# Kernel tuning notes

Hardware: AMD Instinct MI355X
Metric: run time of the kernel (lower is better)

The kernel has to match this reference:

```python
import jax, jax.numpy as jnp
import numpy as np

S, B, D, H = 2048, 2, 1024, 16
DK = D // H


def rotate_half(x):
    # interleaved variant: pairs (x0,x1)->(-x1,x0)
    x1 = x[..., ::2]
    x2 = x[..., 1::2]
    return jnp.stack((-x2, x1), axis=-1).reshape(x.shape)


def apply_rope(x):
    # x: [B, H, S, dk]
    b, h, s, dk = x.shape
    pos = jnp.arange(s, dtype=jnp.float32)
    inv_freq = 1.0 / (10000.0 ** (jnp.arange(0, dk, 2, dtype=jnp.float32) / dk))
    freqs = jnp.einsum('i,j->ij', pos, inv_freq)          # [S, dk/2]
    emb = jnp.concatenate((freqs, freqs), axis=-1)        # [S, dk]  (non-interleaved cos/sin, as in source)
    cos = jnp.cos(emb)[None, None, :, :]
    sin = jnp.sin(emb)[None, None, :, :]
    return x * cos + rotate_half(x) * sin


def setup_inputs() -> dict:
    key = jax.random.key(0)
    ks = jax.random.split(key, 11)
    sc = 0.02
    return {
        'query': jax.random.normal(ks[0], (S, B, D), jnp.float32),
        'key':   jax.random.normal(ks[1], (S, B, D), jnp.float32),
        'value': jax.random.normal(ks[2], (S, B, D), jnp.float32),
        'wq': jax.random.normal(ks[3], (D, D), jnp.float32) * sc,
        'bq': jax.random.normal(ks[4], (D,), jnp.float32) * sc,
        'wk': jax.random.normal(ks[5], (D, D), jnp.float32) * sc,
        'bk': jax.random.normal(ks[6], (D,), jnp.float32) * sc,
        'wv': jax.random.normal(ks[7], (D, D), jnp.float32) * sc,
        'bv': jax.random.normal(ks[8], (D,), jnp.float32) * sc,
        'wo': jax.random.normal(ks[9], (D, D), jnp.float32) * sc,
        'bo': jax.random.normal(ks[10], (D,), jnp.float32) * sc,
    }


def reference(query, key, value, wq, bq, wk, bk, wv, bv, wo, bo):
    s_q, b, _ = query.shape
    s_k = key.shape[0]

    def split_heads(x, s):
        # [S,B,D] -> [B,H,S,dk]
        return x.transpose(1, 0, 2).reshape(b, s, H, DK).transpose(0, 2, 1, 3)

    Q = split_heads(query @ wq.T + bq, s_q)
    K = split_heads(key @ wk.T + bk, s_k)
    V = split_heads(value @ wv.T + bv, s_k)

    Q = apply_rope(Q)
    K = apply_rope(K)

    scores = jnp.einsum('bhqd,bhkd->bhqk', Q, K) / jnp.sqrt(jnp.float32(DK))
    attn = jax.nn.softmax(scores, axis=-1)
    out = jnp.einsum('bhqk,bhkd->bhqd', attn, V)          # [B,H,Sq,dk]
    out = out.transpose(0, 2, 1, 3).reshape(b, s_q, D)    # [B,Sq,D]
    out = out.transpose(1, 0, 2)                          # [Sq,B,D]
    return out @ wo.T + bo
```

## Files before the change

### kernel.cpp

```cpp
#include <hip/hip_runtime.h>
#include <cstdint>
#include <cstddef>

typedef __attribute__((ext_vector_type(4))) float f32x4;
typedef __attribute__((ext_vector_type(8))) float f32x8;
typedef __attribute__((ext_vector_type(16))) float f32x16;
typedef __attribute__((ext_vector_type(8))) __bf16 bf16x8;
typedef __attribute__((ext_vector_type(4))) __bf16 bf16x4;
typedef __attribute__((ext_vector_type(2))) __bf16 bf16x2;
typedef __attribute__((ext_vector_type(4))) unsigned int u32x4;
typedef unsigned short u16;

#define S_LEN 2048
#define BATCH 2
#define DMODEL 1024
#define NHEAD 16
#define HDK 64

__device__ __forceinline__ u16 f2bf(float f) {
    uint32_t u = __float_as_uint(f);
    u += 0x7FFFu + ((u >> 16) & 1u);
    return (u16)(u >> 16);
}

__device__ __forceinline__ void gload_lds16(const void* g, void* l) {
    __builtin_amdgcn_global_load_lds(
        (const __attribute__((address_space(1))) uint32_t*)g,
        (__attribute__((address_space(3))) uint32_t*)l, 16, 0, 0);
}

__device__ __forceinline__ unsigned pk2(float a, float b) {
    bf16x2 t;
    t[0] = (__bf16)a; t[1] = (__bf16)b;
    return __builtin_bit_cast(unsigned, t);
}

__device__ __forceinline__ float fmax3(float a, float b, float c) {
    return fmaxf(fmaxf(a, b), c);
}

__device__ __forceinline__ f32x16 z16() {
    f32x16 v = {0.f,0.f,0.f,0.f,0.f,0.f,0.f,0.f,0.f,0.f,0.f,0.f,0.f,0.f,0.f,0.f};
    return v;
}

__global__ __launch_bounds__(256) void cvt_kernel(
    const float* __restrict__ a0, const float* __restrict__ a1, const float* __restrict__ a2,
    const float* __restrict__ a3, const float* __restrict__ a4, const float* __restrict__ a5,
    const float* __restrict__ a6,
    u16* __restrict__ o0, u16* __restrict__ o1, u16* __restrict__ o2,
    u16* __restrict__ o3, u16* __restrict__ o4, u16* __restrict__ o5,
    u16* __restrict__ o6)
{
    const int by = blockIdx.y;
    const float* s;
    u16* d;
    int n;
    switch (by) {
        case 0: s = a0; d = o0; n = 4194304; break;
        case 1: s = a1; d = o1; n = 4194304; break;
        case 2: s = a2; d = o2; n = 4194304; break;
        case 3: s = a3; d = o3; n = 1048576; break;
        case 4: s = a4; d = o4; n = 1048576; break;
        case 5: s = a5; d = o5; n = 1048576; break;
        default: s = a6; d = o6; n = 1048576; break;
    }
    int idx = (blockIdx.x * 256 + threadIdx.x) * 8;
    if (idx >= n) return;
    float4 f0 = *(const float4*)(s + idx);
    float4 f1 = *(const float4*)(s + idx + 4);
    alignas(16) u16 o[8] = {f2bf(f0.x), f2bf(f0.y), f2bf(f0.z), f2bf(f0.w),
                            f2bf(f1.x), f2bf(f1.y), f2bf(f1.z), f2bf(f1.w)};
    *(u32x4*)(d + idx) = *(const u32x4*)o;
}

__global__ __launch_bounds__(512, 6) void qkv_kernel(
    const u16* __restrict__ X0, const u16* __restrict__ X1, const u16* __restrict__ X2,
    const u16* __restrict__ W0, const u16* __restrict__ W1, const u16* __restrict__ W2,
    const float* __restrict__ B0, const float* __restrict__ B1, const float* __restrict__ B2,
    u16* __restrict__ O0, u16* __restrict__ O1, u16* __restrict__ O2)
{
    __shared__ __align__(16) u16 lA[2][128 * 32];
    __shared__ __align__(16) u16 lB[2][128 * 32];
    const int tid = threadIdx.x, wid = tid >> 6, lane = tid & 63;
    const int l15 = lane & 15, l4 = lane >> 4;
    const int p = blockIdx.y * 32 + blockIdx.x;
    const int vid = (p & 7) * 96 + (p >> 3);
    const int bx = vid & 31, byv = vid >> 5;
    const int mat = byv >> 3;
    const u16* X = mat == 0 ? X0 : (mat == 1 ? X1 : X2);
    const u16* W = mat == 0 ? W0 : (mat == 1 ? W1 : W2);
    const float* bias = mat == 0 ? B0 : (mat == 1 ? B1 : B2);
    u16* O = mat == 0 ? O0 : (mat == 1 ? O1 : O2);
    const int m0 = bx * 128, n0 = (byv & 7) * 128;
    const int mw = (wid >> 1) * 32, nw = (wid & 1) * 64;

    f32x4 acc[2][4];
#pragma unroll
    for (int i = 0; i < 2; ++i)
#pragma unroll
        for (int j = 0; j < 4; ++j) acc[i][j] = (f32x4){0.f, 0.f, 0.f, 0.f};

    const int srow = tid >> 2, sg = (tid & 3) ^ (srow & 3);

#define QSTAGE(bufi, k0_) do {                                                \
        gload_lds16(X + (size_t)(m0 + srow) * 1024 + (k0_) + sg * 8,          \
                    (char*)lA + (bufi) * 8192 + (tid & ~63) * 16);            \
        gload_lds16(W + (size_t)(n0 + srow) * 1024 + (k0_) + sg * 8,          \
                    (char*)lB + (bufi) * 8192 + (tid & ~63) * 16);            \
    } while (0)

    QSTAGE(0, 0);
    for (int ks = 0; ks < 32; ++ks) {
        const int cur = ks & 1;
        if (ks < 31) {
            QSTAGE(cur ^ 1, (ks + 1) * 32);
            asm volatile("s_waitcnt vmcnt(2)" ::: "memory");
        } else {
            asm volatile("s_waitcnt vmcnt(0)" ::: "memory");
        }
        __builtin_amdgcn_s_barrier();
        const char* la = (const char*)lA + cur * 8192;
        const char* lb = (const char*)lB + cur * 8192;
        __builtin_amdgcn_s_setprio(1);
        bf16x8 af[2], bfr[4];
#pragma unroll
        for (int f = 0; f < 2; ++f) {
            int ra = mw + f * 16 + l15;
            af[f] = *(const bf16x8*)(la + ra * 64 +
                    ((l4 * 16) ^ ((ra & 3) << 4)));
        }
#pragma unroll
        for (int f = 0; f < 4; ++f) {
            int rb = nw + f * 16 + l15;
            bfr[f] = *(const bf16x8*)(lb + rb * 64 +
                    ((l4 * 16) ^ ((rb & 3) << 4)));
        }
#pragma unroll
        for (int mf = 0; mf < 2; ++mf)
#pragma unroll
            for (int nf = 0; nf < 4; ++nf)
                acc[mf][nf] = __builtin_amdgcn_mfma_f32_16x16x32_bf16(
                    af[mf], bfr[nf], acc[mf][nf], 0, 0, 0);
        __builtin_amdgcn_s_setprio(0);
        __builtin_amdgcn_s_barrier();
    }
#undef QSTAGE

#pragma unroll
    for (int mf = 0; mf < 2; ++mf) {
#pragma unroll
        for (int nf = 0; nf < 4; ++nf) {
            int gcol = n0 + nw + nf * 16 + l15;
            float bval = bias[gcol];
            int h = gcol >> 6, d = gcol & 63;
            float invf = __expf(-(float)(d & 31) * 0.2878231366f);
#pragma unroll
            for (int i = 0; i < 4; ++i) {
                int grow = m0 + mw + mf * 16 + l4 * 4 + i;
                int s = grow >> 1, b = grow & 1;
                float v = acc[mf][nf][i] + bval;
                if (mat < 2) {
                    float p2 = __shfl_xor(v, 1);
                    float th = (float)s * invf;
                    float sn, cs;
                    __sincosf(th, &sn, &cs);
                    v = (d & 1) ? fmaf(p2, sn, v * cs) : fmaf(-p2, sn, v * cs);
                    if (mat == 0) v *= 0.18033688f;
                }
                O[((size_t)(b * NHEAD + h) * S_LEN + s) * HDK + d] = f2bf(v);
            }
        }
    }
}

__global__ __launch_bounds__(256) void vtrans_kernel(const u16* __restrict__ Vr, u16* __restrict__ Vt)
{
    __shared__ __align__(16) u16 t[64][72];
    const int tid = threadIdx.x, bh = blockIdx.y, s0 = blockIdx.x * 64;
    const u16* src = Vr + (size_t)bh * S_LEN * HDK;
    u16* dst = Vt + (size_t)bh * HDK * S_LEN;
    int r = tid >> 2, cbase = (tid & 3) * 16;
#pragma unroll
    for (int j = 0; j < 2; ++j)
        *(bf16x8*)&t[r][cbase + j * 8] =
            *(const bf16x8*)(const void*)(src + (size_t)(s0 + r) * HDK + cbase + j * 8);
    __syncthreads();
    int d = tid >> 2;
#pragma unroll
    for (int j = 0; j < 2; ++j) {
        alignas(16) u16 tmp[8];
#pragma unroll
        for (int x = 0; x < 8; ++x) {
            int lp = j * 8 + x;
            int sl = (lp & 3) | ((lp & 4) << 1) | ((lp & 8) >> 1);
            tmp[x] = t[cbase + sl][d];
        }
        *(bf16x8*)(void*)(dst + (size_t)d * S_LEN + s0 + cbase + j * 8) = *(const bf16x8*)tmp;
    }
}

__global__ __launch_bounds__(512, 4) void attn_kernel(
    const u16* __restrict__ Q, const u16* __restrict__ K,
    const u16* __restrict__ V, u16* __restrict__ O)
{
    __shared__ __align__(16) char smem[65536];
    const int tid = threadIdx.x, wid = tid >> 6, lane = tid & 63;
    const int g = wid >> 2, wv = wid & 3;
    const int l31 = lane & 31, hi = lane >> 5;
    const int p = blockIdx.y * 16 + blockIdx.x;
    const int vid = (p & 7) * 64 + (p >> 3);
    const int bh = vid >> 4, b = bh >> 4, h = bh & 15;
    const int q0 = (vid & 15) * 128;
    const u16* Qb = Q + (size_t)bh * S_LEN * HDK;
    const u16* Kb = K + (size_t)bh * S_LEN * HDK;
    const u16* Vb = V + (size_t)bh * HDK * S_LEN;

    const int qrow = q0 + wv * 32 + l31;
    bf16x8 aq[4];
#pragma unroll
    for (int ks = 0; ks < 4; ++ks)
        aq[ks] = *(const bf16x8*)(const void*)(Qb + (size_t)qrow * HDK + ks * 16 + hi * 8);

    f32x16 acc0 = z16(), acc1 = z16();
    float mrow = -1e30f, lpart = 0.f;

    char* gbase = smem + g * 32768;
    const int gt = tid & 255;
    const int srow = gt >> 3, lg = (gt & 7) ^ (srow & 7);
    char* sK = gbase + wv * 1024;
    char* sV = gbase + 8192 + wv * 1024;
    const u16* pk0 = Kb + (size_t)(g * 1024 + srow) * HDK + lg * 8;
    const u16* pk1 = pk0 + 32 * HDK;
    const u16* pv0 = Vb + (size_t)srow * S_LEN + g * 1024 + lg * 8;
    const u16* pv1 = pv0 + (size_t)32 * S_LEN;

    const int swl = (l31 & 7) << 4;
    const char* akr[4];
    const char* avr[4];
#pragma unroll
    for (int i = 0; i < 4; ++i) {
        akr[i] = gbase + l31 * 128 + ((i * 32 + hi * 16) ^ swl);
        avr[i] = gbase + 8192 + l31 * 128 + ((i * 32 + hi * 16) ^ swl);
    }

    gload_lds16(pk0, sK);
    gload_lds16(pk1, sK + 4096);
    gload_lds16(pv0, sV);
    gload_lds16(pv1, sV + 4096);
    pk0 += 4096; pk1 += 4096; pv0 += 64; pv1 += 64;

#define TILE(CUR_, STG_) do {                                                 \
    if (STG_) {                                                               \
        gload_lds16(pk0, sK + ((CUR_) ^ 1) * 16384);                          \
        gload_lds16(pk1, sK + ((CUR_) ^ 1) * 16384 + 4096);                   \
        gload_lds16(pv0, sV + ((CUR_) ^ 1) * 16384);                          \
        gload_lds16(pv1, sV + ((CUR_) ^ 1) * 16384 + 4096);                   \
        pk0 += 4096; pk1 += 4096; pv0 += 64; pv1 += 64;                       \
        asm volatile("s_waitcnt vmcnt(4)" ::: "memory");                      \
    } else {                                                                  \
        asm volatile("s_waitcnt vmcnt(0)" ::: "memory");                      \
    }                                                                         \
    __builtin_amdgcn_s_barrier();                                             \
    f32x16 s0 = z16(), s1 = z16();                                            \
    __builtin_amdgcn_s_setprio(1);                                            \
    _Pragma("unroll")                                                         \
    for (int ks = 0; ks < 4; ++ks) {                                          \
        bf16x8 a0 = *(const bf16x8*)(akr[ks] + (CUR_) * 16384);               \
        bf16x8 a1 = *(const bf16x8*)(akr[ks] + (CUR_) * 16384 + 4096);        \
        s0 = __builtin_amdgcn_mfma_f32_32x32x16_bf16(a0, aq[ks], s0, 0, 0, 0);\
        s1 = __builtin_amdgcn_mfma_f32_32x32x16_bf16(a1, aq[ks], s1, 0, 0, 0);\
    }                                                                         \
    __builtin_amdgcn_s_setprio(0);                                            \
    float a0_ = fmax3(s0[0], s0[1], s0[2]);                                   \
    float a1_ = fmax3(s0[3], s0[4], s0[5]);                                   \
    float a2_ = fmax3(s0[6], s0[7], s0[8]);                                   \
    float a3_ = fmax3(s0[9], s0[10], s0[11]);                                 \
    float a4_ = fmax3(s0[12], s0[13], s0[14]);                                \
    float b0_ = fmax3(s1[0], s1[1], s1[2]);                                   \
    float b1_ = fmax3(s1[3], s1[4], s1[5]);                                   \
    float b2_ = fmax3(s1[6], s1[7], s1[8]);                                   \
    float b3_ = fmax3(s1[9], s1[10], s1[11]);                                 \
    float b4_ = fmax3(s1[12], s1[13], s1[14]);                                \
    float t0_ = fmax3(a0_, a1_, a2_);                                         \
    float t1_ = fmax3(a3_, a4_, s0[15]);                                      \
    float t2_ = fmax3(b0_, b1_, b2_);                                         \
    float t3_ = fmax3(b3_, b4_, s1[15]);                                      \
    float pmax = fmaxf(fmax3(t0_, t1_, t2_), t3_);                            \
    pmax = fmaxf(pmax, __shfl_xor(pmax, 32));                                 \
    if (!__all(pmax - mrow <= 11.5f)) {                                       \
        float mn = fmaxf(mrow, pmax);                                         \
        float sc = __builtin_amdgcn_exp2f(mrow - mn);                         \
        lpart *= sc;                                                          \
        acc0 *= sc; acc1 *= sc;                                               \
        mrow = mn;                                                            \
    }                                                                         \
    _Pragma("unroll")                                                         \
    for (int i = 0; i < 16; ++i) {                                            \
        s0[i] = __builtin_amdgcn_exp2f(s0[i] - mrow);                         \
        s1[i] = __builtin_amdgcn_exp2f(s1[i] - mrow);                         \
    }                                                                         \
    {                                                                         \
        f32x16 sm_ = s0 + s1;                                                 \
        f32x8 q8_ = __builtin_shufflevector(sm_, sm_, 0,1,2,3,4,5,6,7)        \
                  + __builtin_shufflevector(sm_, sm_, 8,9,10,11,12,13,14,15); \
        f32x4 q4_ = __builtin_shufflevector(q8_, q8_, 0,1,2,3)                \
                  + __builtin_shufflevector(q8_, q8_, 4,5,6,7);               \
        lpart += (q4_[0] + q4_[1]) + (q4_[2] + q4_[3]);                       \
    }                                                                         \
    __builtin_amdgcn_s_setprio(1);                                            \
    _Pragma("unroll")                                                         \
    for (int i = 0; i < 4; ++i) {                                             \
        const f32x16* cp = (i >> 1) ? &s1 : &s0;                              \
        const int e0 = (i & 1) * 8;                                           \
        u32x4 bw;                                                             \
        bw[0] = pk2((*cp)[e0 + 0], (*cp)[e0 + 1]);                            \
        bw[1] = pk2((*cp)[e0 + 2], (*cp)[e0 + 3]);                            \
        bw[2] = pk2((*cp)[e0 + 4], (*cp)[e0 + 5]);                            \
        bw[3] = pk2((*cp)[e0 + 6], (*cp)[e0 + 7]);                            \
        bf16x8 Bf = __builtin_bit_cast(bf16x8, bw);                           \
        bf16x8 av0 = *(const bf16x8*)(avr[i] + (CUR_) * 16384);               \
        bf16x8 av1 = *(const bf16x8*)(avr[i] + (CUR_) * 16384 + 4096);        \
        acc0 = __builtin_amdgcn_mfma_f32_32x32x16_bf16(av0, Bf, acc0, 0, 0, 0);\
        acc1 = __builtin_amdgcn_mfma_f32_32x32x16_bf16(av1, Bf, acc1, 0, 0, 0);\
    }                                                                         \
    __builtin_amdgcn_s_setprio(0);                                            \
    __builtin_amdgcn_s_barrier();                                             \
} while (0)

    for (int th = 0; th < 8; ++th) {
        TILE(0, 1);
        TILE(1, (th < 7));
    }
#undef TILE

    lpart += __shfl_xor(lpart, 32);
    float* exO = (float*)smem;
    float* exML = (float*)(smem + 36864);
    const int sl = wv * 64 + lane;
    if (g == 1) {
#pragma unroll
        for (int r4 = 0; r4 < 4; ++r4) {
            f32x4 w0 = {acc0[r4 * 4 + 0], acc0[r4 * 4 + 1], acc0[r4 * 4 + 2], acc0[r4 * 4 + 3]};
            f32x4 w1 = {acc1[r4 * 4 + 0], acc1[r4 * 4 + 1], acc1[r4 * 4 + 2], acc1[r4 * 4 + 3]};
            *(f32x4*)(exO + sl * 36 + r4 * 4) = w0;
            *(f32x4*)(exO + sl * 36 + 16 + r4 * 4) = w1;
        }
        exML[sl * 2] = mrow;
        exML[sl * 2 + 1] = lpart;
    }
    __syncthreads();
    if (g == 0) {
        float m1 = exML[sl * 2], l1 = exML[sl * 2 + 1];
        float mm = fmaxf(mrow, m1);
        float f0 = __builtin_amdgcn_exp2f(mrow - mm);
        float f1 = __builtin_amdgcn_exp2f(m1 - mm);
        float rl = 1.0f / (lpart * f0 + l1 * f1);
        f0 *= rl; f1 *= rl;
        u16* obase = O + ((size_t)qrow * BATCH + b) * DMODEL + h * HDK;
#pragma unroll
        for (int db = 0; db < 2; ++db) {
#pragma unroll
            for (int r4 = 0; r4 < 4; ++r4) {
                f32x4 part = *(const f32x4*)(exO + sl * 36 + db * 16 + r4 * 4);
                bf16x4 outv;
#pragma unroll
                for (int e = 0; e < 4; ++e) {
                    float own = db ? acc1[r4 * 4 + e] : acc0[r4 * 4 + e];
                    outv[e] = (__bf16)(own * f0 + part[e] * f1);
                }
                *(bf16x4*)(void*)(obase + db * 32 + 8 * r4 + 4 * hi) = outv;
            }
        }
    }
}

__global__ __launch_bounds__(256) void proj_kernel(
    const u16* __restrict__ A, const u16* __restrict__ W,
    const float* __restrict__ bias, float* __restrict__ out)
{
    __shared__ __align__(16) u16 lA[2][64 * 64];
    __shared__ __align__(16) u16 lB[2][128 * 64];
    const int tid = threadIdx.x, wid = tid >> 6, lane = tid & 63;
    const int l15 = lane & 15, l4 = lane >> 4;
    const int p = blockIdx.y * 8 + blockIdx.x;
    const int vid = (p & 7) * 64 + (p >> 3);
    const int m0 = (vid & 63) * 64, n0 = (vid >> 6) * 128;
    const int nw = wid * 32;

    f32x4 acc[4][2];
#pragma unroll
    for (int i = 0; i < 4; ++i)
#pragma unroll
        for (int j = 0; j < 2; ++j) acc[i][j] = (f32x4){0.f, 0.f, 0.f, 0.f};

#define PSTAGE(bufi, k0_) do {                                                \
        _Pragma("unroll")                                                     \
        for (int it = 0; it < 2; ++it) {                                      \
            int cc = it * 256 + tid;                                          \
            int row = cc >> 3, gg = (cc & 7) ^ (row & 7);                     \
            gload_lds16(A + (size_t)(m0 + row) * 1024 + (k0_) + gg * 8,       \
                        (char*)lA + (bufi) * 8192 + (cc & ~63) * 16);         \
        }                                                                     \
        _Pragma("unroll")                                                     \
        for (int it = 0; it < 4; ++it) {                                      \
            int cc = it * 256 + tid;                                          \
            int row = cc >> 3, gg = (cc & 7) ^ (row & 7);                     \
            gload_lds16(W + (size_t)(n0 + row) * 1024 + (k0_) + gg * 8,       \
                        (char*)lB + (bufi) * 16384 + (cc & ~63) * 16);        \
        }                                                                     \
    } while (0)

    PSTAGE(0, 0);
    for (int ks = 0; ks < 16; ++ks) {
        const int cur = ks & 1;
        if (ks < 15) {
            PSTAGE(cur ^ 1, (ks + 1) * 64);
            asm volatile("s_waitcnt vmcnt(6)" ::: "memory");
        } else {
            asm volatile("s_waitcnt vmcnt(0)" ::: "memory");
        }
        __builtin_amdgcn_s_barrier();
        const char* la = (const char*)lA + cur * 8192;
        const char* lb = (const char*)lB + cur * 16384;
        __builtin_amdgcn_s_setprio(1);
#pragma unroll
        for (int kk = 0; kk < 2; ++kk) {
            bf16x8 af[4], bfr[2];
#pragma unroll
            for (int f = 0; f < 4; ++f) {
                int ra = f * 16 + l15;
                af[f] = *(const bf16x8*)(la + ra * 128 +
                        ((kk * 64 + l4 * 16) ^ ((ra & 7) << 4)));
            }
#pragma unroll
            for (int f = 0; f < 2; ++f) {
                int rb = nw + f * 16 + l15;
                bfr[f] = *(const bf16x8*)(lb + rb * 128 +
                        ((kk * 64 + l4 * 16) ^ ((rb & 7) << 4)));
            }
#pragma unroll
            for (int mf = 0; mf < 4; ++mf)
#pragma unroll
                for (int nf = 0; nf < 2; ++nf)
                    acc[mf][nf] = __builtin_amdgcn_mfma_f32_16x16x32_bf16(
                        af[mf], bfr[nf], acc[mf][nf], 0, 0, 0);
        }
        __builtin_amdgcn_s_setprio(0);
        __builtin_amdgcn_s_barrier();
    }
#undef PSTAGE

#pragma unroll
    for (int mf = 0; mf < 4; ++mf) {
#pragma unroll
        for (int nf = 0; nf < 2; ++nf) {
            int gcol = n0 + nw + nf * 16 + l15;
            float bval = bias[gcol];
#pragma unroll
            for (int i = 0; i < 4; ++i) {
                int grow = m0 + mf * 16 + l4 * 4 + i;
                out[(size_t)grow * DMODEL + gcol] = acc[mf][nf][i] + bval;
            }
        }
    }
}

extern "C" void kernel_launch(void* const* d_in, const int* in_sizes, int n_in,
                              void* d_out, int out_size, void* d_ws, size_t ws_size,
                              hipStream_t stream)
{
    (void)in_sizes; (void)n_in; (void)out_size; (void)ws_size;
    const float* q  = (const float*)d_in[0];
    const float* k  = (const float*)d_in[1];
    const float* v  = (const float*)d_in[2];
    const float* wq = (const float*)d_in[3];
    const float* bq = (const float*)d_in[4];
    const float* wk = (const float*)d_in[5];
    const float* bk = (const float*)d_in[6];
    const float* wv = (const float*)d_in[7];
    const float* bv = (const float*)d_in[8];
    const float* wo = (const float*)d_in[9];
    const float* bo = (const float*)d_in[10];

    char* ws = (char*)d_ws;
    const size_t MB = 1024 * 1024;
    u16* XQ  = (u16*)(ws + 0 * MB);
    u16* XK  = (u16*)(ws + 8 * MB);
    u16* XV  = (u16*)(ws + 16 * MB);
    u16* WQb = (u16*)(ws + 24 * MB);
    u16* WKb = (u16*)(ws + 26 * MB);
    u16* WVb = (u16*)(ws + 28 * MB);
    u16* WOb = (u16*)(ws + 30 * MB);
    u16* QR  = (u16*)(ws + 32 * MB);
    u16* KR  = (u16*)(ws + 40 * MB);
    u16* VR  = (u16*)(ws + 48 * MB);
    u16* VT  = XK;
    u16* OA  = XQ;

    cvt_kernel<<<dim3(2048, 7), 256, 0, stream>>>(q, k, v, wq, wk, wv, wo,
                                                  XQ, XK, XV, WQb, WKb, WVb, WOb);
    qkv_kernel<<<dim3(32, 24), 512, 0, stream>>>(XQ, XK, XV, WQb, WKb, WVb,
                                                 bq, bk, bv, QR, KR, VR);
    vtrans_kernel<<<dim3(32, 32), 256, 0, stream>>>(VR, VT);
    attn_kernel<<<dim3(16, 32), 512, 0, stream>>>(QR, KR, VT, OA);
    proj_kernel<<<dim3(8, 64), 256, 0, stream>>>(OA, WOb, bo, (float*)d_out);
}
```

Before: 125.1 us.

## Drop intra-block KV split in attention and use post-exp lazy rescaling

The attention kernel no longer splits the KV sequence between two 4-wave groups in a 512-thread block. Each 256-thread block now walks the whole KV length, which removes the cross-group LDS merge and its block-wide sync and halves shared memory per block. The online softmax now exponentiates scores against a fixed running offset first, and rescales only when a tile's exponentiated max exceeds a threshold, using a reciprocal and log2. In exchange, each block runs twice as many serial KV tiles with half the waves, so per-block latency rises. The new rescaling scheme also carries overflow and precision risk if scores jump by a large amount within a single tile.

After: 129.0 us. +3.0%, slower.

```diff
diff --git a/kernel.cpp b/kernel.cpp
--- a/kernel.cpp
+++ b/kernel.cpp
@@ -200,13 +200,12 @@
     }
 }
 
-__global__ __launch_bounds__(512, 4) void attn_kernel(
+__global__ __launch_bounds__(256) void attn_kernel(
     const u16* __restrict__ Q, const u16* __restrict__ K,
     const u16* __restrict__ V, u16* __restrict__ O)
 {
-    __shared__ __align__(16) char smem[65536];
+    __shared__ __align__(16) char smem[32768];
     const int tid = threadIdx.x, wid = tid >> 6, lane = tid & 63;
-    const int g = wid >> 2, wv = wid & 3;
     const int l31 = lane & 31, hi = lane >> 5;
     const int p = blockIdx.y * 16 + blockIdx.x;
     const int vid = (p & 7) * 64 + (p >> 3);
@@ -216,23 +215,21 @@
     const u16* Kb = K + (size_t)bh * S_LEN * HDK;
     const u16* Vb = V + (size_t)bh * HDK * S_LEN;
 
-    const int qrow = q0 + wv * 32 + l31;
+    const int qrow = q0 + wid * 32 + l31;
     bf16x8 aq[4];
 #pragma unroll
     for (int ks = 0; ks < 4; ++ks)
         aq[ks] = *(const bf16x8*)(const void*)(Qb + (size_t)qrow * HDK + ks * 16 + hi * 8);
 
     f32x16 acc0 = z16(), acc1 = z16();
-    float mrow = -1e30f, lpart = 0.f;
-
-    char* gbase = smem + g * 32768;
-    const int gt = tid & 255;
-    const int srow = gt >> 3, lg = (gt & 7) ^ (srow & 7);
-    char* sK = gbase + wv * 1024;
-    char* sV = gbase + 8192 + wv * 1024;
-    const u16* pk0 = Kb + (size_t)(g * 1024 + srow) * HDK + lg * 8;
+    float mrow = 0.0f, lpart = 0.f;
+
+    const int srow = tid >> 3, lg = (tid & 7) ^ (srow & 7);
+    char* sK = smem + wid * 1024;
+    char* sV = smem + 8192 + wid * 1024;
+    const u16* pk0 = Kb + (size_t)srow * HDK + lg * 8;
     const u16* pk1 = pk0 + 32 * HDK;
-    const u16* pv0 = Vb + (size_t)srow * S_LEN + g * 1024 + lg * 8;
+    const u16* pv0 = Vb + (size_t)srow * S_LEN + lg * 8;
     const u16* pv1 = pv0 + (size_t)32 * S_LEN;
 
     const int swl = (l31 & 7) << 4;
@@ -240,8 +237,8 @@
     const char* avr[4];
 #pragma unroll
     for (int i = 0; i < 4; ++i) {
-        akr[i] = gbase + l31 * 128 + ((i * 32 + hi * 16) ^ swl);
-        avr[i] = gbase + 8192 + l31 * 128 + ((i * 32 + hi * 16) ^ swl);
+        akr[i] = smem + l31 * 128 + ((i * 32 + hi * 16) ^ swl);
+        avr[i] = smem + 8192 + l31 * 128 + ((i * 32 + hi * 16) ^ swl);
     }
 
     gload_lds16(pk0, sK);
@@ -272,6 +269,11 @@
         s1 = __builtin_amdgcn_mfma_f32_32x32x16_bf16(a1, aq[ks], s1, 0, 0, 0);\
     }                                                                         \
     __builtin_amdgcn_s_setprio(0);                                            \
+    _Pragma("unroll")                                                         \
+    for (int i = 0; i < 16; ++i) {                                            \
+        s0[i] = __builtin_amdgcn_exp2f(s0[i] - mrow);                         \
+        s1[i] = __builtin_amdgcn_exp2f(s1[i] - mrow);                         \
+    }                                                                         \
     float a0_ = fmax3(s0[0], s0[1], s0[2]);                                   \
     float a1_ = fmax3(s0[3], s0[4], s0[5]);                                   \
     float a2_ = fmax3(s0[6], s0[7], s0[8]);                                   \
@@ -288,17 +290,13 @@
     float t3_ = fmax3(b3_, b4_, s1[15]);                                      \
     float pmax = fmaxf(fmax3(t0_, t1_, t2_), t3_);                            \
     pmax = fmaxf(pmax, __shfl_xor(pmax, 32));                                 \
-    if (!__all(pmax - mrow <= 11.5f)) {                                       \
-        float mn = fmaxf(mrow, pmax);                                         \
-        float sc = __builtin_amdgcn_exp2f(mrow - mn);                         \
+    if (!__all(pmax <= 2896.3f)) {                 \
+        float sc = 1.0f / pmax;                                               \
+        mrow += __log2f(pmax);                                                \
         lpart *= sc;                                                          \
         acc0 *= sc; acc1 *= sc;                                               \
-        mrow = mn;                                                            \
-    }                                                                         \
-    _Pragma("unroll")                                                         \
-    for (int i = 0; i < 16; ++i) {                                            \
-        s0[i] = __builtin_amdgcn_exp2f(s0[i] - mrow);                         \
-        s1[i] = __builtin_amdgcn_exp2f(s1[i] - mrow);                         \
+        _Pragma("unroll")                                                     \
+        for (int i = 0; i < 16; ++i) { s0[i] *= sc; s1[i] *= sc; }            \
     }                                                                         \
     {                                                                         \
         f32x16 sm_ = s0 + s1;                                                 \
@@ -328,49 +326,26 @@
     __builtin_amdgcn_s_barrier();                                             \
 } while (0)
 
-    for (int th = 0; th < 8; ++th) {
+    for (int th = 0; th < 16; ++th) {
         TILE(0, 1);
-        TILE(1, (th < 7));
+        TILE(1, (th < 15));
     }
 #undef TILE
 
     lpart += __shfl_xor(lpart, 32);
-    float* exO = (float*)smem;
-    float* exML = (float*)(smem + 36864);
-    const int sl = wv * 64 + lane;
-    if (g == 1) {
+    float rl = 1.0f / lpart;
+    u16* obase = O + ((size_t)qrow * BATCH + b) * DMODEL + h * HDK;
+#pragma unroll
+    for (int db = 0; db < 2; ++db) {
 #pragma unroll
         for (int r4 = 0; r4 < 4; ++r4) {
-            f32x4 w0 = {acc0[r4 * 4 + 0], acc0[r4 * 4 + 1], acc0[r4 * 4 + 2], acc0[r4 * 4 + 3]};
-            f32x4 w1 = {acc1[r4 * 4 + 0], acc1[r4 * 4 + 1], acc1[r4 * 4 + 2], acc1[r4 * 4 + 3]};
-            *(f32x4*)(exO + sl * 36 + r4 * 4) = w0;
-            *(f32x4*)(exO + sl * 36 + 16 + r4 * 4) = w1;
-        }
-        exML[sl * 2] = mrow;
-        exML[sl * 2 + 1] = lpart;
-    }
-    __syncthreads();
-    if (g == 0) {
-        float m1 = exML[sl * 2], l1 = exML[sl * 2 + 1];
-        float mm = fmaxf(mrow, m1);
-        float f0 = __builtin_amdgcn_exp2f(mrow - mm);
-        float f1 = __builtin_amdgcn_exp2f(m1 - mm);
-        float rl = 1.0f / (lpart * f0 + l1 * f1);
-        f0 *= rl; f1 *= rl;
-        u16* obase = O + ((size_t)qrow * BATCH + b) * DMODEL + h * HDK;
-#pragma unroll
-        for (int db = 0; db < 2; ++db) {
-#pragma unroll
-            for (int r4 = 0; r4 < 4; ++r4) {
-                f32x4 part = *(const f32x4*)(exO + sl * 36 + db * 16 + r4 * 4);
-                bf16x4 outv;
-#pragma unroll
-                for (int e = 0; e < 4; ++e) {
-                    float own = db ? acc1[r4 * 4 + e] : acc0[r4 * 4 + e];
-                    outv[e] = (__bf16)(own * f0 + part[e] * f1);
-                }
-                *(bf16x4*)(void*)(obase + db * 32 + 8 * r4 + 4 * hi) = outv;
+            bf16x4 outv;
+#pragma unroll
+            for (int e = 0; e < 4; ++e) {
+                float own = db ? acc1[r4 * 4 + e] : acc0[r4 * 4 + e];
+                outv[e] = (__bf16)(own * rl);
             }
+            *(bf16x4*)(void*)(obase + db * 32 + 8 * r4 + 4 * hi) = outv;
         }
     }
 }
@@ -503,6 +478,6 @@
     qkv_kernel<<<dim3(32, 24), 512, 0, stream>>>(XQ, XK, XV, WQb, WKb, WVb,
                                                  bq, bk, bv, QR, KR, VR);
     vtrans_kernel<<<dim3(32, 32), 256, 0, stream>>>(VR, VT);
-    attn_kernel<<<dim3(16, 32), 512, 0, stream>>>(QR, KR, VT, OA);
+    attn_kernel<<<dim3(16, 32), 256, 0, stream>>>(QR, KR, VT, OA);
     proj_kernel<<<dim3(8, 64), 256, 0, stream>>>(OA, WOb, bo, (float*)d_out);
 }
```
